# Optimization experiments

Measured on AMD Instinct MI355X. Metric: run time of the kernel, lower is better.

## Reference

```python
import jax, jax.numpy as jnp
import numpy as np

N, E, F_IN, C1, H1, C2, NUM_CLASSES, NUM_GRAPHS = 50000, 800000, 128, 64, 4, 128, 5, 32
NEG_SLOPE = 0.2


def gat_conv(x, W, att_src, att_dst, bias, src, dst, heads, out_ch):
    # x: [N, in], W: [in, heads*out_ch], att_*: [heads, out_ch], bias: [heads*out_ch]
    n = x.shape[0]
    h = (x @ W).reshape(n, heads, out_ch)                      # [N,H,C]
    a_src = jnp.sum(h * att_src, axis=-1)                      # [N,H]
    a_dst = jnp.sum(h * att_dst, axis=-1)                      # [N,H]
    alpha = a_src[src] + a_dst[dst]                            # [E,H]
    alpha = jax.nn.leaky_relu(alpha, NEG_SLOPE)
    # scatter-softmax over incoming edges of each dst node (every node has a self-loop)
    amax = jax.ops.segment_max(alpha, dst, num_segments=n)
    ealpha = jnp.exp(alpha - amax[dst])
    denom = jax.ops.segment_sum(ealpha, dst, num_segments=n)
    alpha = ealpha / (denom[dst] + 1e-16)                      # [E,H]
    msg = h[src] * alpha[..., None]                            # [E,H,C]
    out = jax.ops.segment_sum(msg, dst, num_segments=n)        # [N,H,C]
    return out.reshape(n, heads * out_ch) + bias


def setup_inputs() -> dict:
    key = jax.random.key(0)
    ks = jax.random.split(key, 12)
    x = jax.random.normal(ks[0], (N, F_IN), dtype=jnp.float32)
    edge_index = jax.random.randint(ks[1], (2, E), 0, N, dtype=jnp.int64)
    batch = jnp.sort(jax.random.randint(ks[2], (N,), 0, NUM_GRAPHS, dtype=jnp.int64))
    s1 = 1.0 / np.sqrt(F_IN)
    s2 = 1.0 / np.sqrt(H1 * C1)
    s3 = 1.0 / np.sqrt(C2)
    return {
        "x": x,
        "edge_index": edge_index,
        "batch": batch,
        "W1": jax.random.normal(ks[3], (F_IN, H1 * C1), dtype=jnp.float32) * s1,
        "att_src1": jax.random.normal(ks[4], (H1, C1), dtype=jnp.float32) * s1,
        "att_dst1": jax.random.normal(ks[5], (H1, C1), dtype=jnp.float32) * s1,
        "b1": jnp.zeros((H1 * C1,), dtype=jnp.float32),
        "W2": jax.random.normal(ks[6], (H1 * C1, C2), dtype=jnp.float32) * s2,
        "att_src2": jax.random.normal(ks[7], (1, C2), dtype=jnp.float32) * s2,
        "att_dst2": jax.random.normal(ks[8], (1, C2), dtype=jnp.float32) * s2,
        "b2": jnp.zeros((C2,), dtype=jnp.float32),
        "lin_w": jax.random.normal(ks[9], (C2, NUM_CLASSES), dtype=jnp.float32) * s3,
        "lin_b": jnp.zeros((NUM_CLASSES,), dtype=jnp.float32),
    }


def reference(x, edge_index, batch, W1, att_src1, att_dst1, b1, W2, att_src2, att_dst2, b2, lin_w, lin_b):
    n = x.shape[0]
    # PyG GATConv adds self-loops by default
    loops = jnp.arange(n, dtype=edge_index.dtype)
    src = jnp.concatenate([edge_index[0], loops])
    dst = jnp.concatenate([edge_index[1], loops])
    h = jax.nn.elu(gat_conv(x, W1, att_src1, att_dst1, b1, src, dst, H1, C1))
    h = jax.nn.elu(gat_conv(h, W2, att_src2, att_dst2, b2, src, dst, 1, C2))
    # global_mean_pool over graphs
    sums = jax.ops.segment_sum(h, batch, num_segments=NUM_GRAPHS)          # [G,C2]
    counts = jax.ops.segment_sum(jnp.ones((n,), h.dtype), batch, num_segments=NUM_GRAPHS)
    pooled = sums / jnp.maximum(counts, 1.0)[:, None]
    # dropout is identity in eval mode
    return pooled @ lin_w + lin_b
```

## Files before the change

### kernel.cpp

```cpp
#include <hip/hip_runtime.h>
#include <math.h>

#define NEG_SLOPE 0.2f

__device__ inline float lrelu(float x) { return x > 0.f ? x : NEG_SLOPE * x; }

typedef __attribute__((ext_vector_type(8))) _Float16 f16x8;
typedef __attribute__((ext_vector_type(4))) float f32x4;
typedef __attribute__((ext_vector_type(2))) float f32x2;
typedef __attribute__((ext_vector_type(4))) _Float16 h16x4;
typedef __attribute__((ext_vector_type(2))) _Float16 h16x2;

__global__ void convW_k(const float* __restrict__ W1, const float* __restrict__ W2,
                        _Float16* __restrict__ BT1, _Float16* __restrict__ BT2)
{
    int i = blockIdx.x * blockDim.x + threadIdx.x;
    if (i < 32768) {
        int n = i >> 7, k = i & 127;
        BT1[(size_t)n * 128 + k] = (_Float16)W1[(size_t)k * 256 + n];
    } else {
        int idx = i - 32768;
        int n = idx >> 8, k = idx & 255;
        BT2[(size_t)n * 256 + k] = (_Float16)W2[(size_t)k * 128 + n];
    }
}

template<int N, int K, int H, bool AF16>
__launch_bounds__(256)
__global__ void gemm_fused(const void* __restrict__ A, const _Float16* __restrict__ BT,
                           unsigned char* __restrict__ HB, const float* __restrict__ att_s,
                           const float* __restrict__ att_d, float* __restrict__ aS,
                           float* __restrict__ aD, int M)
{
    constexpr int ITERS = K / 32;
    constexpr int WN = N / 4;
    constexpr int NT = WN / 16;
    constexpr int NCH = (N * 4) / 256;
    __shared__ unsigned short As[64 * 40] __attribute__((aligned(16)));
    __shared__ unsigned short Bs[N * 40] __attribute__((aligned(16)));
    const int t = threadIdx.x;
    const int wave = t >> 6, lane = t & 63;
    const int quad = lane >> 4, l15 = lane & 15;
    const int rowBase = blockIdx.x * 64;

    f32x4 acc[4][NT];
#pragma unroll
    for (int mi = 0; mi < 4; ++mi)
#pragma unroll
        for (int ni = 0; ni < NT; ++ni)
            acc[mi][ni] = (f32x4){0.f, 0.f, 0.f, 0.f};

    const int ar = t >> 2;
    const int ak = (t & 3) << 3;
    const int bc = (t * NCH) >> 2;
    const int bks = (t * NCH) & 3;

    for (int it = 0; it < ITERS; ++it) {
        {
            int gr = rowBase + ar;
            f16x8 hv;
#pragma unroll
            for (int j = 0; j < 8; ++j) hv[j] = (_Float16)0.f;
            if (gr < M) {
                if constexpr (AF16) {
                    hv = *(const f16x8*)((const _Float16*)A + (size_t)gr * K + it * 32 + ak);
                } else {
                    const float* ap = (const float*)A + (size_t)gr * K + it * 32 + ak;
                    float4 v0 = *(const float4*)ap;
                    float4 v1 = *(const float4*)(ap + 4);
                    hv[0] = (_Float16)v0.x; hv[1] = (_Float16)v0.y;
                    hv[2] = (_Float16)v0.z; hv[3] = (_Float16)v0.w;
                    hv[4] = (_Float16)v1.x; hv[5] = (_Float16)v1.y;
                    hv[6] = (_Float16)v1.z; hv[7] = (_Float16)v1.w;
                }
            }
            *(f16x8*)&As[ar * 40 + ak] = hv;
        }
        {
            const _Float16* bp = BT + (size_t)bc * K + it * 32 + bks * 8;
            unsigned short* dp = &Bs[bc * 40 + bks * 8];
#pragma unroll
            for (int j = 0; j < NCH; ++j)
                *(f16x8*)(dp + j * 8) = *(const f16x8*)(bp + j * 8);
        }
        __syncthreads();
        f16x8 af[4], bfr[NT];
#pragma unroll
        for (int mi = 0; mi < 4; ++mi)
            af[mi] = *(const f16x8*)&As[(mi * 16 + l15) * 40 + quad * 8];
#pragma unroll
        for (int ni = 0; ni < NT; ++ni)
            bfr[ni] = *(const f16x8*)&Bs[(wave * WN + ni * 16 + l15) * 40 + quad * 8];
#pragma unroll
        for (int mi = 0; mi < 4; ++mi)
#pragma unroll
            for (int ni = 0; ni < NT; ++ni)
                acc[mi][ni] = __builtin_amdgcn_mfma_f32_16x16x32_f16(
                    af[mi], bfr[ni], acc[mi][ni], 0, 0, 0);
        __syncthreads();
    }
    float asv[NT], adv[NT];
#pragma unroll
    for (int ni = 0; ni < NT; ++ni) {
        int col = wave * WN + ni * 16 + l15;
        asv[ni] = att_s[col];
        adv[ni] = att_d[col];
    }
#pragma unroll
    for (int mi = 0; mi < 4; ++mi) {
#pragma unroll
        for (int r = 0; r < 4; ++r) {
            int row = rowBase + mi * 16 + quad * 4 + r;
            bool ok = row < M;
            float ss = 0.f, sd = 0.f;
#pragma unroll
            for (int ni = 0; ni < NT; ++ni) {
                float v = acc[mi][ni][r];
                ss += v * asv[ni];
                sd += v * adv[ni];
            }
#pragma unroll
            for (int ni = 0; ni < NT; ni += 2) {
                int pk = __builtin_amdgcn_cvt_pk_fp8_f32(acc[mi][ni][r],
                                                         acc[mi][ni + 1][r], 0, false);
                if (ok) {
                    HB[(size_t)row * N + wave * WN + ni * 16 + l15] =
                        (unsigned char)(pk & 0xff);
                    HB[(size_t)row * N + wave * WN + (ni + 1) * 16 + l15] =
                        (unsigned char)((pk >> 8) & 0xff);
                }
            }
#pragma unroll
            for (int off = 8; off > 0; off >>= 1) {
                ss += __shfl_xor(ss, off);
                sd += __shfl_xor(sd, off);
            }
            if (ok && l15 == 0) {
                if (H == 4) {
                    aS[row * 4 + wave] = ss;
                    aD[row * 4 + wave] = sd;
                } else {
                    atomicAdd(&aS[row], ss);
                    atomicAdd(&aD[row], sd);
                }
            }
        }
    }
}

#define BIN_EPT 32
__launch_bounds__(256)
__global__ void bcount_k(const int* __restrict__ dst, int* __restrict__ bcnt,
                         int ET, int E, int NBUCK)
{
    __shared__ int hist[1024];
    for (int i = threadIdx.x; i < NBUCK; i += 256) hist[i] = 0;
    __syncthreads();
    int e0 = blockIdx.x * (256 * BIN_EPT) + threadIdx.x;
#pragma unroll
    for (int j = 0; j < BIN_EPT; ++j) {
        int e = e0 + j * 256;
        if (e < ET) {
            int d = (e < E) ? dst[e] : (e - E);
            atomicAdd(&hist[d >> 6], 1);
        }
    }
    __syncthreads();
    for (int i = threadIdx.x; i < NBUCK; i += 256) {
        int c = hist[i];
        if (c > 0) atomicAdd(&bcnt[i], c);
    }
}

__global__ void bscan_k(const int* __restrict__ bcnt, int* __restrict__ bbase,
                        int* __restrict__ ccursor, int nb)
{
    __shared__ int sh[1024];
    int t = threadIdx.x;
    int v = (t < nb) ? bcnt[t] : 0;
    sh[t] = v;
    __syncthreads();
#pragma unroll
    for (int o = 1; o < 1024; o <<= 1) {
        int u = (t >= o) ? sh[t - o] : 0;
        __syncthreads();
        sh[t] += u;
        __syncthreads();
    }
    if (t < nb) {
        int excl = sh[t] - v;
        bbase[t] = excl;
        ccursor[t] = excl;
    }
    if (t == nb - 1) bbase[nb] = sh[t];
}

__launch_bounds__(256)
__global__ void binpass_k(const int* __restrict__ src, const int* __restrict__ dst,
                          int* __restrict__ ccursor, unsigned int* __restrict__ tmp,
                          int ET, int E, int NBUCK)
{
    __shared__ int hist[1024];
    for (int i = threadIdx.x; i < NBUCK; i += 256) hist[i] = 0;
    __syncthreads();
    int e0 = blockIdx.x * (256 * BIN_EPT) + threadIdx.x;
    unsigned int ev[BIN_EPT];
    int meta[BIN_EPT];
#pragma unroll
    for (int j = 0; j < BIN_EPT; ++j) {
        int e = e0 + j * 256;
        meta[j] = -1;
        if (e < ET) {
            int s, d;
            if (e < E) { s = src[e]; d = dst[e]; } else { s = e - E; d = s; }
            ev[j] = (unsigned int)s | ((unsigned int)d << 16);
            int b = d >> 6;
            int r = atomicAdd(&hist[b], 1);
            meta[j] = (r << 10) | b;
        }
    }
    __syncthreads();
    for (int i = threadIdx.x; i < NBUCK; i += 256) {
        int c = hist[i];
        hist[i] = (c > 0) ? atomicAdd(&ccursor[i], c) : 0;
    }
    __syncthreads();
#pragma unroll
    for (int j = 0; j < BIN_EPT; ++j) {
        if (meta[j] >= 0) {
            int b = meta[j] & 1023;
            int r = meta[j] >> 10;
            tmp[hist[b] + r] = ev[j];
        }
    }
}

__global__ void fine_k(const int* __restrict__ bbase, const unsigned int* __restrict__ tmp,
                       int* __restrict__ rowptr, unsigned short* __restrict__ esrc,
                       int Nn, int ET, int NBUCK)
{
    __shared__ int lcnt[64], lpre[64], lcur[64];
    int t = threadIdx.x;
    int b = blockIdx.x;
    int n0 = b << 6;
    int base = bbase[b];
    int end = bbase[b + 1];
    if (t < 64) lcnt[t] = 0;
    __syncthreads();
    for (int i = base + t; i < end; i += 256)
        atomicAdd(&lcnt[(tmp[i] >> 16) & 63], 1);
    __syncthreads();
    if (t < 64) lpre[t] = lcnt[t];
    __syncthreads();
#pragma unroll
    for (int o = 1; o < 64; o <<= 1) {
        int u = (t < 64 && t >= o) ? lpre[t - o] : 0;
        __syncthreads();
        if (t < 64) lpre[t] += u;
        __syncthreads();
    }
    if (t < 64) {
        int n = n0 + t;
        int excl = lpre[t] - lcnt[t];
        if (n < Nn) {
            rowptr[n] = base + excl;
            lcur[t] = base + excl;
        }
    }
    if (b == NBUCK - 1 && t == 0) rowptr[Nn] = ET;
    __syncthreads();
    for (int i = base + t; i < end; i += 256) {
        unsigned int v = tmp[i];
        int pos = atomicAdd(&lcur[(v >> 16) & 63], 1);
        esrc[pos] = (unsigned short)(v & 0xffffu);
    }
}

template<int H>
__global__ void alpha_k(const int* __restrict__ rp, const unsigned short* __restrict__ esrc,
                        const float* __restrict__ aS, const float* __restrict__ aD,
                        _Float16* __restrict__ wout, int ET, int Nn)
{
    int d = blockIdx.x * 4 + (threadIdx.x >> 6);
    int lane = threadIdx.x & 63;
    if (d >= Nn) return;
    int p0 = __builtin_amdgcn_readfirstlane(rp[d]);
    int p1 = __builtin_amdgcn_readfirstlane(rp[d + 1]);
    float adh[H];
#pragma unroll
    for (int h = 0; h < H; ++h) adh[h] = aD[d * H + h];
    float m[H];
#pragma unroll
    for (int h = 0; h < H; ++h) m[h] = -1e30f;
    for (int p = p0 + lane; p < p1; p += 64) {
        int s = esrc[p];
        if (H == 4) {
            float4 a4 = *(const float4*)&aS[s * 4];
            m[0] = fmaxf(m[0], lrelu(a4.x + adh[0]));
            m[1] = fmaxf(m[1], lrelu(a4.y + adh[1]));
            m[2] = fmaxf(m[2], lrelu(a4.z + adh[2]));
            m[3] = fmaxf(m[3], lrelu(a4.w + adh[3]));
        } else {
            m[0] = fmaxf(m[0], lrelu(aS[s] + adh[0]));
        }
    }
#pragma unroll
    for (int h = 0; h < H; ++h)
#pragma unroll
        for (int off = 32; off > 0; off >>= 1)
            m[h] = fmaxf(m[h], __shfl_xor(m[h], off));
    for (int p = p0 + lane; p < p1; p += 64) {
        int s = esrc[p];
        if (H == 4) {
            float4 a4 = *(const float4*)&aS[s * 4];
            wout[p] = (_Float16)__expf(lrelu(a4.x + adh[0]) - m[0]);
            wout[(size_t)ET + p] = (_Float16)__expf(lrelu(a4.y + adh[1]) - m[1]);
            wout[(size_t)2 * ET + p] = (_Float16)__expf(lrelu(a4.z + adh[2]) - m[2]);
            wout[(size_t)3 * ET + p] = (_Float16)__expf(lrelu(a4.w + adh[3]) - m[3]);
        } else {
            wout[p] = (_Float16)__expf(lrelu(aS[s] + adh[0]) - m[0]);
        }
    }
}

__global__ void gather1_k(const int* __restrict__ rp, const unsigned short* __restrict__ esrc,
                          const unsigned char* __restrict__ hb, const _Float16* __restrict__ wv,
                          const float* __restrict__ bias, _Float16* __restrict__ out,
                          int ET, int Nn)
{
    int d = blockIdx.x * 4 + (threadIdx.x >> 6);
    int lane = threadIdx.x & 63;
    if (d >= Nn) return;
    int c4 = lane << 2;
    const _Float16* wh = wv + (size_t)(lane >> 4) * ET;
    int p0 = __builtin_amdgcn_readfirstlane(rp[d]);
    int p1 = __builtin_amdgcn_readfirstlane(rp[d + 1]);
    float den = 0.f;
    float ax = 0.f, ay = 0.f, az = 0.f, aw = 0.f;
    int p = p0;
    for (; p + 8 <= p1; p += 8) {
        int s[8];
#pragma unroll
        for (int j = 0; j < 8; ++j) s[j] = __builtin_amdgcn_readfirstlane(esrc[p + j]);
        unsigned int v[8];
#pragma unroll
        for (int j = 0; j < 8; ++j)
            v[j] = *(const unsigned int*)&hb[(size_t)s[j] * 256 + c4];
        float w[8];
#pragma unroll
        for (int j = 0; j < 8; ++j) w[j] = (float)wh[p + j];
#pragma unroll
        for (int j = 0; j < 8; ++j) {
            den += w[j];
            f32x2 lo = __builtin_amdgcn_cvt_pk_f32_fp8((int)v[j], false);
            f32x2 hi = __builtin_amdgcn_cvt_pk_f32_fp8((int)v[j], true);
            ax += lo[0] * w[j];
            ay += lo[1] * w[j];
            az += hi[0] * w[j];
            aw += hi[1] * w[j];
        }
    }
    int rem = p1 - p;
    if (rem > 0) {
        int s[8];
        unsigned int v[8];
        float w[8];
#pragma unroll
        for (int j = 0; j < 8; ++j)
            if (j < rem) s[j] = __builtin_amdgcn_readfirstlane(esrc[p + j]);
#pragma unroll
        for (int j = 0; j < 8; ++j)
            if (j < rem) v[j] = *(const unsigned int*)&hb[(size_t)s[j] * 256 + c4];
#pragma unroll
        for (int j = 0; j < 8; ++j)
            if (j < rem) w[j] = (float)wh[p + j];
#pragma unroll
        for (int j = 0; j < 8; ++j) {
            if (j < rem) {
                den += w[j];
                f32x2 lo = __builtin_amdgcn_cvt_pk_f32_fp8((int)v[j], false);
                f32x2 hi = __builtin_amdgcn_cvt_pk_f32_fp8((int)v[j], true);
                ax += lo[0] * w[j];
                ay += lo[1] * w[j];
                az += hi[0] * w[j];
                aw += hi[1] * w[j];
            }
        }
    }
    float inv = 1.f / (den + 1e-16f);
    float4 b4 = *(const float4*)&bias[c4];
    float rx, ry, rz, rw;
    rx = ax * inv + b4.x; rx = rx > 0.f ? rx : expm1f(rx);
    ry = ay * inv + b4.y; ry = ry > 0.f ? ry : expm1f(ry);
    rz = az * inv + b4.z; rz = rz > 0.f ? rz : expm1f(rz);
    rw = aw * inv + b4.w; rw = rw > 0.f ? rw : expm1f(rw);
    h16x4 r16;
    r16[0] = (_Float16)rx; r16[1] = (_Float16)ry;
    r16[2] = (_Float16)rz; r16[3] = (_Float16)rw;
    *(h16x4*)&out[(size_t)d * 256 + c4] = r16;
}

__global__ void gather2_k(const int* __restrict__ rp, const unsigned short* __restrict__ esrc,
                          const unsigned char* __restrict__ hb, const _Float16* __restrict__ wv,
                          _Float16* __restrict__ out, int ET, int Nn)
{
    int d = blockIdx.x * 4 + (threadIdx.x >> 6);
    int lane = threadIdx.x & 63;
    if (d >= Nn) return;
    int c2 = lane << 1;
    int p0 = __builtin_amdgcn_readfirstlane(rp[d]);
    int p1 = __builtin_amdgcn_readfirstlane(rp[d + 1]);
    float den = 0.f;
    float ax = 0.f, ay = 0.f;
    int p = p0;
    for (; p + 8 <= p1; p += 8) {
        int s[8];
#pragma unroll
        for (int j = 0; j < 8; ++j) s[j] = __builtin_amdgcn_readfirstlane(esrc[p + j]);
        unsigned short v[8];
#pragma unroll
        for (int j = 0; j < 8; ++j)
            v[j] = *(const unsigned short*)&hb[(size_t)s[j] * 128 + c2];
        float w[8];
#pragma unroll
        for (int j = 0; j < 8; ++j) w[j] = (float)wv[p + j];
#pragma unroll
        for (int j = 0; j < 8; ++j) {
            den += w[j];
            f32x2 lo = __builtin_amdgcn_cvt_pk_f32_fp8((int)v[j], false);
            ax += lo[0] * w[j];
            ay += lo[1] * w[j];
        }
    }
    int rem = p1 - p;
    if (rem > 0) {
        int s[8];
        unsigned short v[8];
        float w[8];
#pragma unroll
        for (int j = 0; j < 8; ++j)
            if (j < rem) s[j] = __builtin_amdgcn_readfirstlane(esrc[p + j]);
#pragma unroll
        for (int j = 0; j < 8; ++j)
            if (j < rem) v[j] = *(const unsigned short*)&hb[(size_t)s[j] * 128 + c2];
#pragma unroll
        for (int j = 0; j < 8; ++j)
            if (j < rem) w[j] = (float)wv[p + j];
#pragma unroll
        for (int j = 0; j < 8; ++j) {
            if (j < rem) {
                den += w[j];
                f32x2 lo = __builtin_amdgcn_cvt_pk_f32_fp8((int)v[j], false);
                ax += lo[0] * w[j];
                ay += lo[1] * w[j];
            }
        }
    }
    float inv = 1.f / (den + 1e-16f);
    h16x2 r16;
    r16[0] = (_Float16)(ax * inv);
    r16[1] = (_Float16)(ay * inv);
    *(h16x2*)&out[(size_t)d * 128 + c2] = r16;
}

__global__ void pool_k(const _Float16* __restrict__ o2, const float* __restrict__ b2,
                       const int* __restrict__ batch, float* __restrict__ sums, int Nn, int C)
{
    int c = threadIdx.x;
    int n0 = blockIdx.x * 64;
    int n1 = min(n0 + 64, Nn);
    float local = 0.f;
    int gcur = batch[n0];
    float bc = b2[c];
    for (int n = n0; n < n1; ++n) {
        int g = batch[n];
        if (g != gcur) {
            atomicAdd(&sums[gcur * C + c], local);
            local = 0.f;
            gcur = g;
        }
        float v = (float)o2[(size_t)n * C + c] + bc;
        local += v > 0.f ? v : expm1f(v);
    }
    atomicAdd(&sums[gcur * C + c], local);
}

__global__ void final_k(const float* __restrict__ sums, const int* __restrict__ batch,
                        const float* __restrict__ lin_w, const float* __restrict__ lin_b,
                        float* __restrict__ out, int Nn, int G, int C, int NC)
{
    __shared__ float inv[64];
    int t = threadIdx.x;
    if (t < G) {
        int lo = 0, hi = Nn;
        while (lo < hi) { int mid = (lo + hi) >> 1; if (batch[mid] < t) lo = mid + 1; else hi = mid; }
        int lb = lo;
        lo = 0; hi = Nn;
        while (lo < hi) { int mid = (lo + hi) >> 1; if (batch[mid] < t + 1) lo = mid + 1; else hi = mid; }
        int cnt = lo - lb;
        inv[t] = 1.f / fmaxf((float)cnt, 1.f);
    }
    __syncthreads();
    if (t < G * NC) {
        int g = t / NC, k = t % NC;
        float acc = 0.f;
        for (int c = 0; c < C; ++c) acc += sums[g * C + c] * lin_w[c * NC + k];
        out[t] = acc * inv[g] + lin_b[k];
    }
}

extern "C" void kernel_launch(void* const* d_in, const int* in_sizes, int n_in,
                              void* d_out, int out_size, void* d_ws, size_t ws_size,
                              hipStream_t stream)
{
    const float* x      = (const float*)d_in[0];
    const int*   eidx   = (const int*)d_in[1];
    const int*   batch  = (const int*)d_in[2];
    const float* W1     = (const float*)d_in[3];
    const float* att_s1 = (const float*)d_in[4];
    const float* att_d1 = (const float*)d_in[5];
    const float* b1     = (const float*)d_in[6];
    const float* W2     = (const float*)d_in[7];
    const float* att_s2 = (const float*)d_in[8];
    const float* att_d2 = (const float*)d_in[9];
    const float* b2     = (const float*)d_in[10];
    const float* lin_w  = (const float*)d_in[11];
    const float* lin_b  = (const float*)d_in[12];

    const int Nn  = in_sizes[2];
    const int E   = in_sizes[1] / 2;
    const int H1_ = 4, C1_ = 64, C2_ = 128, G = 32, NC = 5;
    const int D1 = H1_ * C1_;
    const int ET = E + Nn;
    const int NBUCK = (Nn + 63) >> 6;

    const int* srcp = eidx;
    const int* dstp = eidx + E;

    float* ws = (float*)d_ws;
    size_t off = 0;
    auto alloc = [&](size_t n) { float* p = ws + off; off += n; return p; };
    _Float16* o1h = (_Float16*)alloc((size_t)Nn * D1 / 2);
    _Float16* o2h = (_Float16*)alloc((size_t)Nn * C2_ / 2);
    float* aS1  = alloc((size_t)Nn * H1_);
    float* aD1  = alloc((size_t)Nn * H1_);
    float* aS2  = alloc(Nn);
    float* aD2  = alloc(Nn);
    float* sums = alloc((size_t)G * C2_);
    _Float16* BT1 = (_Float16*)alloc(D1 * 128 / 2);
    _Float16* BT2 = (_Float16*)alloc(C2_ * 256 / 2);
    unsigned char* hb1 = (unsigned char*)alloc((size_t)Nn * D1 / 4);
    unsigned char* hb2 = (unsigned char*)alloc((size_t)Nn * C2_ / 4);
    _Float16* w1h = (_Float16*)alloc((size_t)2 * ET + 16);
    _Float16* w2h = (_Float16*)alloc((size_t)ET / 2 + 16);
    int* iws    = (int*)(ws + off);
    int* rowptr = iws;
    int* bcnt   = iws + Nn + 1;
    int* bbase  = iws + Nn + 1 + 1024;
    int* ccursor= iws + Nn + 1 + 2049;
    unsigned int* tmp = (unsigned int*)(iws + Nn + 1 + 2049 + 1024);
    unsigned short* esrc = (unsigned short*)(tmp + ET);

    const int GB = (Nn + 63) / 64;
    const int NW = (Nn + 3) / 4;
    const int BINB = (ET + 256 * BIN_EPT - 1) / (256 * BIN_EPT);

    hipMemsetAsync(bcnt, 0, 1024 * 4, stream);
    hipMemsetAsync(aS2, 0, (size_t)2 * Nn * 4, stream);
    bcount_k<<<BINB, 256, 0, stream>>>(dstp, bcnt, ET, E, NBUCK);
    bscan_k<<<1, 1024, 0, stream>>>(bcnt, bbase, ccursor, NBUCK);
    binpass_k<<<BINB, 256, 0, stream>>>(srcp, dstp, ccursor, tmp, ET, E, NBUCK);
    fine_k<<<NBUCK, 256, 0, stream>>>(bbase, tmp, rowptr, esrc, Nn, ET, NBUCK);

    convW_k<<<256, 256, 0, stream>>>(W1, W2, BT1, BT2);

    gemm_fused<256, 128, 4, false><<<GB, 256, 0, stream>>>(x, BT1, hb1, att_s1, att_d1,
                                                           aS1, aD1, Nn);
    alpha_k<4><<<NW, 256, 0, stream>>>(rowptr, esrc, aS1, aD1, w1h, ET, Nn);
    gather1_k<<<NW, 256, 0, stream>>>(rowptr, esrc, hb1, w1h, b1, o1h, ET, Nn);

    gemm_fused<128, 256, 1, true><<<GB, 256, 0, stream>>>(o1h, BT2, hb2, att_s2, att_d2,
                                                          aS2, aD2, Nn);
    alpha_k<1><<<NW, 256, 0, stream>>>(rowptr, esrc, aS2, aD2, w2h, ET, Nn);
    gather2_k<<<NW, 256, 0, stream>>>(rowptr, esrc, hb2, w2h, o2h, ET, Nn);

    hipMemsetAsync(sums, 0, (size_t)G * C2_ * 4, stream);
    pool_k<<<GB, C2_, 0, stream>>>(o2h, b2, batch, sums, Nn, C2_);
    final_k<<<1, 256, 0, stream>>>(sums, batch, lin_w, lin_b, (float*)d_out, Nn, G, C2_, NC);
}
```

Measured before the change: 354.0 us.

## Fuse attention softmax weights into gather kernels, dropping max pass

Removes both alpha_k kernels, which computed per-edge exponentiated attention weights and wrote them to fp16 buffers. The gather kernels now compute exp(leaky_relu(aS[src]+aD[dst])) inline from the per-node attention scores they already index by source. This eliminates two edge-level passes, the weight buffers' write and read traffic, and two kernel launches. In exchange, each lane recomputes the exponential redundantly within a head. The softmax also skips subtracting the segment max, so large attention logits could overflow fp32 exp.

Result: faster. 324.5 us (-8.3%).

```diff
diff --git a/kernel.cpp b/kernel.cpp
--- a/kernel.cpp
+++ b/kernel.cpp
@@ -276,65 +276,20 @@
     }
 }
 
-template<int H>
-__global__ void alpha_k(const int* __restrict__ rp, const unsigned short* __restrict__ esrc,
-                        const float* __restrict__ aS, const float* __restrict__ aD,
-                        _Float16* __restrict__ wout, int ET, int Nn)
-{
-    int d = blockIdx.x * 4 + (threadIdx.x >> 6);
-    int lane = threadIdx.x & 63;
-    if (d >= Nn) return;
-    int p0 = __builtin_amdgcn_readfirstlane(rp[d]);
-    int p1 = __builtin_amdgcn_readfirstlane(rp[d + 1]);
-    float adh[H];
-#pragma unroll
-    for (int h = 0; h < H; ++h) adh[h] = aD[d * H + h];
-    float m[H];
-#pragma unroll
-    for (int h = 0; h < H; ++h) m[h] = -1e30f;
-    for (int p = p0 + lane; p < p1; p += 64) {
-        int s = esrc[p];
-        if (H == 4) {
-            float4 a4 = *(const float4*)&aS[s * 4];
-            m[0] = fmaxf(m[0], lrelu(a4.x + adh[0]));
-            m[1] = fmaxf(m[1], lrelu(a4.y + adh[1]));
-            m[2] = fmaxf(m[2], lrelu(a4.z + adh[2]));
-            m[3] = fmaxf(m[3], lrelu(a4.w + adh[3]));
-        } else {
-            m[0] = fmaxf(m[0], lrelu(aS[s] + adh[0]));
-        }
-    }
-#pragma unroll
-    for (int h = 0; h < H; ++h)
-#pragma unroll
-        for (int off = 32; off > 0; off >>= 1)
-            m[h] = fmaxf(m[h], __shfl_xor(m[h], off));
-    for (int p = p0 + lane; p < p1; p += 64) {
-        int s = esrc[p];
-        if (H == 4) {
-            float4 a4 = *(const float4*)&aS[s * 4];
-            wout[p] = (_Float16)__expf(lrelu(a4.x + adh[0]) - m[0]);
-            wout[(size_t)ET + p] = (_Float16)__expf(lrelu(a4.y + adh[1]) - m[1]);
-            wout[(size_t)2 * ET + p] = (_Float16)__expf(lrelu(a4.z + adh[2]) - m[2]);
-            wout[(size_t)3 * ET + p] = (_Float16)__expf(lrelu(a4.w + adh[3]) - m[3]);
-        } else {
-            wout[p] = (_Float16)__expf(lrelu(aS[s] + adh[0]) - m[0]);
-        }
-    }
-}
-
 __global__ void gather1_k(const int* __restrict__ rp, const unsigned short* __restrict__ esrc,
-                          const unsigned char* __restrict__ hb, const _Float16* __restrict__ wv,
-                          const float* __restrict__ bias, _Float16* __restrict__ out,
-                          int ET, int Nn)
+                          const unsigned char* __restrict__ hb, const float* __restrict__ aS,
+                          const float* __restrict__ aD, const float* __restrict__ bias,
+                          _Float16* __restrict__ out, int Nn)
 {
     int d = blockIdx.x * 4 + (threadIdx.x >> 6);
     int lane = threadIdx.x & 63;
     if (d >= Nn) return;
     int c4 = lane << 2;
-    const _Float16* wh = wv + (size_t)(lane >> 4) * ET;
+    int head = lane >> 4;
     int p0 = __builtin_amdgcn_readfirstlane(rp[d]);
     int p1 = __builtin_amdgcn_readfirstlane(rp[d + 1]);
+    float adh = aD[d * 4 + head];
+    const float* aSh = aS + head;
     float den = 0.f;
     float ax = 0.f, ay = 0.f, az = 0.f, aw = 0.f;
     int p = p0;
@@ -348,7 +303,7 @@
             v[j] = *(const unsigned int*)&hb[(size_t)s[j] * 256 + c4];
         float w[8];
 #pragma unroll
-        for (int j = 0; j < 8; ++j) w[j] = (float)wh[p + j];
+        for (int j = 0; j < 8; ++j) w[j] = __expf(lrelu(aSh[s[j] * 4] + adh));
 #pragma unroll
         for (int j = 0; j < 8; ++j) {
             den += w[j];
@@ -373,7 +328,7 @@
             if (j < rem) v[j] = *(const unsigned int*)&hb[(size_t)s[j] * 256 + c4];
 #pragma unroll
         for (int j = 0; j < 8; ++j)
-            if (j < rem) w[j] = (float)wh[p + j];
+            if (j < rem) w[j] = __expf(lrelu(aSh[s[j] * 4] + adh));
 #pragma unroll
         for (int j = 0; j < 8; ++j) {
             if (j < rem) {
@@ -401,8 +356,8 @@
 }
 
 __global__ void gather2_k(const int* __restrict__ rp, const unsigned short* __restrict__ esrc,
-                          const unsigned char* __restrict__ hb, const _Float16* __restrict__ wv,
-                          _Float16* __restrict__ out, int ET, int Nn)
+                          const unsigned char* __restrict__ hb, const float* __restrict__ aS,
+                          const float* __restrict__ aD, _Float16* __restrict__ out, int Nn)
 {
     int d = blockIdx.x * 4 + (threadIdx.x >> 6);
     int lane = threadIdx.x & 63;
@@ -410,6 +365,7 @@
     int c2 = lane << 1;
     int p0 = __builtin_amdgcn_readfirstlane(rp[d]);
     int p1 = __builtin_amdgcn_readfirstlane(rp[d + 1]);
+    float adh = aD[d];
     float den = 0.f;
     float ax = 0.f, ay = 0.f;
     int p = p0;
@@ -423,7 +379,7 @@
             v[j] = *(const unsigned short*)&hb[(size_t)s[j] * 128 + c2];
         float w[8];
 #pragma unroll
-        for (int j = 0; j < 8; ++j) w[j] = (float)wv[p + j];
+        for (int j = 0; j < 8; ++j) w[j] = __expf(lrelu(aS[s[j]] + adh));
 #pragma unroll
         for (int j = 0; j < 8; ++j) {
             den += w[j];
@@ -445,7 +401,7 @@
             if (j < rem) v[j] = *(const unsigned short*)&hb[(size_t)s[j] * 128 + c2];
 #pragma unroll
         for (int j = 0; j < 8; ++j)
-            if (j < rem) w[j] = (float)wv[p + j];
+            if (j < rem) w[j] = __expf(lrelu(aS[s[j]] + adh));
 #pragma unroll
         for (int j = 0; j < 8; ++j) {
             if (j < rem) {
@@ -551,8 +507,6 @@
     _Float16* BT2 = (_Float16*)alloc(C2_ * 256 / 2);
     unsigned char* hb1 = (unsigned char*)alloc((size_t)Nn * D1 / 4);
     unsigned char* hb2 = (unsigned char*)alloc((size_t)Nn * C2_ / 4);
-    _Float16* w1h = (_Float16*)alloc((size_t)2 * ET + 16);
-    _Float16* w2h = (_Float16*)alloc((size_t)ET / 2 + 16);
     int* iws    = (int*)(ws + off);
     int* rowptr = iws;
     int* bcnt   = iws + Nn + 1;
@@ -576,13 +530,11 @@
 
     gemm_fused<256, 128, 4, false><<<GB, 256, 0, stream>>>(x, BT1, hb1, att_s1, att_d1,
                                                            aS1, aD1, Nn);
-    alpha_k<4><<<NW, 256, 0, stream>>>(rowptr, esrc, aS1, aD1, w1h, ET, Nn);
-    gather1_k<<<NW, 256, 0, stream>>>(rowptr, esrc, hb1, w1h, b1, o1h, ET, Nn);
+    gather1_k<<<NW, 256, 0, stream>>>(rowptr, esrc, hb1, aS1, aD1, b1, o1h, Nn);
 
     gemm_fused<128, 256, 1, true><<<GB, 256, 0, stream>>>(o1h, BT2, hb2, att_s2, att_d2,
                                                           aS2, aD2, Nn);
-    alpha_k<1><<<NW, 256, 0, stream>>>(rowptr, esrc, aS2, aD2, w2h, ET, Nn);
-    gather2_k<<<NW, 256, 0, stream>>>(rowptr, esrc, hb2, w2h, o2h, ET, Nn);
+    gather2_k<<<NW, 256, 0, stream>>>(rowptr, esrc, hb2, aS2, aD2, o2h, Nn);
 
     hipMemsetAsync(sums, 0, (size_t)G * C2_ * 4, stream);
     pool_k<<<GB, C2_, 0, stream>>>(o2h, b2, batch, sums, Nn, C2_);
```
